# Kernel optimization log

Hardware: AMD Instinct MI355X
Metric: run time of the kernel (lower is better)

Reference implementation:

```python
import jax, jax.numpy as jnp
import numpy as np

N_NODES = 100000
N_EDGES = 3200000
N_FEAT = 512
N_HID = 256
N_CLASS = 40
K_HOPS = 10


def setup_inputs() -> dict:
    key = jax.random.key(0)
    ks = jax.random.split(key, 8)
    feature = jax.random.normal(ks[0], (N_NODES, N_FEAT), dtype=jnp.float32)
    edge_row = jax.random.randint(ks[1], (N_EDGES,), 0, N_NODES, dtype=jnp.int32)
    edge_col = jax.random.randint(ks[2], (N_EDGES,), 0, N_NODES, dtype=jnp.int32)
    edge_weight = jax.random.uniform(ks[3], (N_EDGES,), dtype=jnp.float32)
    W1 = jax.random.normal(ks[4], (N_FEAT, N_HID), dtype=jnp.float32) * (1.0 / np.sqrt(N_FEAT))
    b1 = jnp.zeros((N_HID,), dtype=jnp.float32)
    W2 = jax.random.normal(ks[5], (N_HID, N_CLASS), dtype=jnp.float32) * (1.0 / np.sqrt(N_HID))
    b2 = jnp.zeros((N_CLASS,), dtype=jnp.float32)
    Wa = jax.random.normal(ks[6], (N_CLASS, 1), dtype=jnp.float32) * (1.0 / np.sqrt(N_CLASS))
    ba = jnp.zeros((1,), dtype=jnp.float32)
    return {"feature": feature, "edge_row": edge_row, "edge_col": edge_col,
            "edge_weight": edge_weight, "W1": W1, "b1": b1, "W2": W2, "b2": b2,
            "Wa": Wa, "ba": ba}


def reference(feature, edge_row, edge_col, edge_weight, W1, b1, W2, b2, Wa, ba):
    # eval mode: dropout is identity
    x = jax.nn.relu(feature @ W1 + b1)          # [N, H]
    x = x @ W2 + b2                              # [N, C]
    # k-hop sparse propagation: out[i] = sum_e w_e * x[col_e] for row_e == i
    xs = [x]
    for _ in range(K_HOPS):
        x = jax.ops.segment_sum(edge_weight[:, None] * x[edge_col], edge_row,
                                num_segments=N_NODES)
        xs.append(x)
    xs = jnp.stack(xs, axis=1)                   # [N, K+1, C]
    score = jax.nn.sigmoid(jnp.squeeze(xs @ Wa + ba, -1))  # [N, K+1]
    out = jnp.einsum('nk,nkc->nc', score, xs)    # attention-weighted hop sum
    return jax.nn.log_softmax(out, axis=1)
```

## Files before the change

kernel.cpp:

```cpp
#include <hip/hip_runtime.h>
#include <math.h>

#define N_NODES 100000
#define N_EDGES 3200000
#define N_FEAT  512
#define N_HID   256
#define N_CLASS 40
#define K_HOPS  10

#define CAP        80
#define NGROUP     8
#define ROWS_PER_G (N_NODES / NGROUP)

typedef __attribute__((ext_vector_type(8))) short short8;
typedef __attribute__((ext_vector_type(8))) unsigned short ushort8v;
typedef __attribute__((ext_vector_type(4))) float float4v;

__device__ inline short f2bf(float f)
{
    union { float f; unsigned u; } v; v.f = f;
    unsigned r = v.u + 0x7FFF + ((v.u >> 16) & 1);
    return (short)(r >> 16);
}

__device__ inline float bf2f(unsigned short u)
{
    union { unsigned u; float f; } v; v.u = (unsigned)u << 16;
    return v.f;
}

__global__ void pack_w1(const float* __restrict__ W1, short* __restrict__ W1p)
{
    const int id = blockIdx.x * 256 + threadIdx.x;
    const int kb = id >> 8, n = id & 255;
    short tmp[32];
#pragma unroll
    for (int kl = 0; kl < 32; ++kl)
        tmp[kl] = f2bf(W1[(size_t)(kb * 32 + kl) * N_HID + n]);
    short8* dst = (short8*)&W1p[id * 32];
#pragma unroll
    for (int j = 0; j < 4; ++j) dst[j] = *(short8*)&tmp[j * 8];
}

__global__ void pack_w2(const float* __restrict__ W2, short* __restrict__ W2p)
{
    const int id = blockIdx.x * 256 + threadIdx.x;
    if (id >= 8 * 48) return;
    const int kb = id / 48, n = id % 48;
    short tmp[32];
#pragma unroll
    for (int kl = 0; kl < 32; ++kl)
        tmp[kl] = (n < N_CLASS) ? f2bf(W2[(size_t)(kb * 32 + kl) * N_CLASS + n]) : (short)0;
    short8* dst = (short8*)&W2p[id * 32];
#pragma unroll
    for (int j = 0; j < 4; ++j) dst[j] = *(short8*)&tmp[j * 8];
}

__global__ __launch_bounds__(256) void mlp_mfma(
    const float* __restrict__ feat, const short* __restrict__ W1p,
    const float* __restrict__ b1, const short* __restrict__ W2p,
    const float* __restrict__ b2, unsigned short* __restrict__ x0)
{
    __shared__ __align__(16) short smem[64 * 264];
    short (*As)[40]  = (short(*)[40])smem;
    short (*Hs)[264] = (short(*)[264])smem;

    const int t    = threadIdx.x;
    const int wave = t >> 6;
    const int lane = t & 63;
    const int q    = lane >> 4;
    const int m    = lane & 15;
    const int n0   = blockIdx.x * 64;
    const int colbase = wave * 64;

    float4v acc[4][4];
#pragma unroll
    for (int i = 0; i < 4; ++i)
#pragma unroll
        for (int j = 0; j < 4; ++j) acc[i][j] = (float4v)0.f;

    for (int kb = 0; kb < 16; ++kb) {
        const int k0 = kb * 32;
        __syncthreads();
        {
            const int r  = t >> 2;
            const int kq = t & 3;
            const int n  = n0 + r;
            float f[8];
            if (n < N_NODES) {
                const float* p = &feat[(size_t)n * N_FEAT + k0 + 8 * kq];
                float4 v0 = *(const float4*)p;
                float4 v1 = *(const float4*)(p + 4);
                f[0]=v0.x; f[1]=v0.y; f[2]=v0.z; f[3]=v0.w;
                f[4]=v1.x; f[5]=v1.y; f[6]=v1.z; f[7]=v1.w;
            } else {
#pragma unroll
                for (int j = 0; j < 8; ++j) f[j] = 0.f;
            }
            short8 st;
#pragma unroll
            for (int j = 0; j < 8; ++j) st[j] = f2bf(f[j]);
            *(short8*)&As[r][8 * kq] = st;
        }
        __syncthreads();

        short8 af[4], bfr[4];
#pragma unroll
        for (int rt = 0; rt < 4; ++rt)
            af[rt] = *(const short8*)&As[rt * 16 + m][q * 8];
#pragma unroll
        for (int ct = 0; ct < 4; ++ct) {
            const int off = (kb * 256 + colbase + ct * 16 + m) * 32 + q * 8;
            bfr[ct] = *(const short8*)&W1p[off];
        }
#pragma unroll
        for (int rt = 0; rt < 4; ++rt)
#pragma unroll
            for (int ct = 0; ct < 4; ++ct)
                acc[rt][ct] = __builtin_amdgcn_mfma_f32_16x16x32_bf16(
                    af[rt], bfr[ct], acc[rt][ct], 0, 0, 0);
    }

    __syncthreads();
#pragma unroll
    for (int ct = 0; ct < 4; ++ct) {
        const int col = colbase + ct * 16 + m;
        const float bias = b1[col];
#pragma unroll
        for (int rt = 0; rt < 4; ++rt) {
            const float4v d = acc[rt][ct];
#pragma unroll
            for (int r = 0; r < 4; ++r) {
                const float hv = fmaxf(d[r] + bias, 0.f);
                Hs[rt * 16 + q * 4 + r][col] = f2bf(hv);
            }
        }
    }
    __syncthreads();

    float4v acc2[3];
#pragma unroll
    for (int ct = 0; ct < 3; ++ct) acc2[ct] = (float4v)0.f;
#pragma unroll
    for (int kb = 0; kb < 8; ++kb) {
        const short8 a2 = *(const short8*)&Hs[wave * 16 + m][kb * 32 + q * 8];
#pragma unroll
        for (int ct = 0; ct < 3; ++ct) {
            const int off = (kb * 48 + ct * 16 + m) * 32 + q * 8;
            const short8 b2f = *(const short8*)&W2p[off];
            acc2[ct] = __builtin_amdgcn_mfma_f32_16x16x32_bf16(a2, b2f, acc2[ct], 0, 0, 0);
        }
    }
#pragma unroll
    for (int ct = 0; ct < 3; ++ct) {
        const int col = ct * 16 + m;
        if (col < N_CLASS) {
            const float bias = b2[col];
#pragma unroll
            for (int r = 0; r < 4; ++r) {
                const int row = n0 + wave * 16 + q * 4 + r;
                if (row < N_NODES)
                    x0[(size_t)row * N_CLASS + col] = (unsigned short)f2bf(acc2[ct][r] + bias);
            }
        }
    }
}

__global__ __launch_bounds__(256) void build_kernel(
    const int* __restrict__ erow, const int* __restrict__ ecol,
    const float* __restrict__ ew, int* __restrict__ cnt,
    unsigned int* __restrict__ ebuck)
{
    const int g     = blockIdx.x & 7;
    const int chunk = blockIdx.x >> 3;
    const int t     = chunk * 256 + threadIdx.x;
    const int base  = t * 16;
    if (base >= N_EDGES) return;
    const int rlo = g * ROWS_PER_G;

#pragma unroll
    for (int qv = 0; qv < 4; ++qv) {
        const int4 r = *(const int4*)&erow[base + qv * 4];
        const int rr[4] = {r.x, r.y, r.z, r.w};
#pragma unroll
        for (int j = 0; j < 4; ++j) {
            const unsigned d = (unsigned)(rr[j] - rlo);
            if (d < (unsigned)ROWS_PER_G) {
                const int   i   = base + qv * 4 + j;
                const int   col = ecol[i];
                const float w   = ew[i];
                int w15 = (int)(w * 32767.f + 0.5f);
                if (w15 > 32767) w15 = 32767;
                const unsigned rec = ((unsigned)w15 << 17) | (unsigned)col;
                const int pos = atomicAdd(&cnt[rr[j]], 1);
                if (pos < CAP)
                    ebuck[(size_t)rr[j] * CAP + pos] = rec;
            }
        }
    }
}

__device__ inline float wave_sum(float v)
{
#pragma unroll
    for (int o = 32; o; o >>= 1) v += __shfl_xor(v, o);
    return v;
}

__global__ __launch_bounds__(256) void attend0_kernel(
    const unsigned short* __restrict__ x, const float* __restrict__ Wa,
    const float* __restrict__ ba, float* __restrict__ acc)
{
    const int lane = threadIdx.x & 63;
    const int row  = blockIdx.x * 4 + (threadIdx.x >> 6);
    if (row >= N_NODES) return;
    const int  c   = lane;
    const bool act = c < N_CLASS;
    const float v  = act ? bf2f(x[(size_t)row * N_CLASS + c]) : 0.f;
    const float tt = act ? v * Wa[c] : 0.f;
    const float z  = wave_sum(tt) + ba[0];
    const float sc = 1.f / (1.f + expf(-z));
    if (act) acc[(size_t)row * N_CLASS + c] = sc * v;
}

__global__ __launch_bounds__(256) void hop_kernel(
    const int* __restrict__ cnt, const unsigned int* __restrict__ ebuck,
    const unsigned short* __restrict__ xin,
    unsigned short* __restrict__ xout, float* __restrict__ acc,
    const float* __restrict__ Wa, const float* __restrict__ ba)
{
    const int lane = threadIdx.x & 63;
    const int row  = blockIdx.x * 4 + (threadIdx.x >> 6);
    if (row >= N_NODES) return;
    const int  slot = lane >> 3;
    const int  l    = lane & 7;
    const bool act  = l < 5;

    int n = cnt[row];
    if (n > CAP) n = CAP;
    const size_t ebase = (size_t)row * CAP;

    unsigned rec_a = (lane < n) ? ebuck[ebase + lane] : 0u;

    float s[8];
#pragma unroll
    for (int j = 0; j < 8; ++j) s[j] = 0.f;

    const int nmain = (n < 64) ? n : 64;
    for (int e = 0; e < nmain; e += 8) {
        const unsigned r = __shfl(rec_a, e + slot);
        const int   col  = (int)(r & 0x1FFFFu);
        const float w    = (float)(r >> 17) * (1.f / 32767.f);
        if (act) {
            const ushort8v v = *(const ushort8v*)&xin[(size_t)col * N_CLASS + l * 8];
#pragma unroll
            for (int j = 0; j < 8; ++j) s[j] += w * bf2f(v[j]);
        }
    }
    for (int e = 64; e < n; e += 8) {
        const int ee = e + slot;
        unsigned r = 0u;
        if (ee < n) r = ebuck[ebase + ee];
        const int   col = (int)(r & 0x1FFFFu);
        const float w   = (float)(r >> 17) * (1.f / 32767.f);
        if (act) {
            const ushort8v v = *(const ushort8v*)&xin[(size_t)col * N_CLASS + l * 8];
#pragma unroll
            for (int j = 0; j < 8; ++j) s[j] += w * bf2f(v[j]);
        }
    }

#pragma unroll
    for (int o = 8; o <= 32; o <<= 1)
#pragma unroll
        for (int j = 0; j < 8; ++j) s[j] += __shfl_xor(s[j], o);

    float tq = 0.f;
    if (act) {
#pragma unroll
        for (int j = 0; j < 8; ++j) tq += s[j] * Wa[l * 8 + j];
    }
#pragma unroll
    for (int o = 1; o <= 4; o <<= 1) tq += __shfl_xor(tq, o);
    const float z  = tq + ba[0];
    const float sc = 1.f / (1.f + expf(-z));

    if (act && slot == 0) {
        ushort8v ov;
#pragma unroll
        for (int j = 0; j < 8; ++j) ov[j] = (unsigned short)f2bf(s[j]);
        *(ushort8v*)&xout[(size_t)row * N_CLASS + l * 8] = ov;

        float4* ap0 = (float4*)&acc[(size_t)row * N_CLASS + l * 8];
        float4 a0 = ap0[0];
        float4 a1 = ap0[1];
        a0.x += sc * s[0]; a0.y += sc * s[1]; a0.z += sc * s[2]; a0.w += sc * s[3];
        a1.x += sc * s[4]; a1.y += sc * s[5]; a1.z += sc * s[6]; a1.w += sc * s[7];
        ap0[0] = a0;
        ap0[1] = a1;
    }
}

__global__ __launch_bounds__(256) void logsoftmax_kernel(
    const float* __restrict__ acc, float* __restrict__ out)
{
    const int lane = threadIdx.x & 63;
    const int row  = blockIdx.x * 4 + (threadIdx.x >> 6);
    if (row >= N_NODES) return;
    const int  c   = lane;
    const bool act = c < N_CLASS;

    float v = act ? acc[(size_t)row * N_CLASS + c] : -INFINITY;
    float mx = v;
#pragma unroll
    for (int o = 32; o; o >>= 1) mx = fmaxf(mx, __shfl_xor(mx, o));
    const float e = act ? expf(v - mx) : 0.f;
    const float s = wave_sum(e);
    if (act) out[(size_t)row * N_CLASS + c] = v - mx - logf(s);
}

extern "C" void kernel_launch(void* const* d_in, const int* in_sizes, int n_in,
                              void* d_out, int out_size, void* d_ws, size_t ws_size,
                              hipStream_t stream)
{
    (void)in_sizes; (void)n_in; (void)out_size; (void)ws_size;
    const float* feat = (const float*)d_in[0];
    const int*   erow = (const int*)d_in[1];
    const int*   ecol = (const int*)d_in[2];
    const float* ew   = (const float*)d_in[3];
    const float* W1   = (const float*)d_in[4];
    const float* b1   = (const float*)d_in[5];
    const float* W2   = (const float*)d_in[6];
    const float* b2   = (const float*)d_in[7];
    const float* Wa   = (const float*)d_in[8];
    const float* ba   = (const float*)d_in[9];
    float* out = (float*)d_out;

    char* ws = (char*)d_ws;
    size_t off = 0;
    auto take = [&](size_t bytes) -> char* {
        char* p = ws + off;
        off += (bytes + 255) & ~(size_t)255;
        return p;
    };
    unsigned short* xb0 = (unsigned short*)take((size_t)N_NODES * N_CLASS * 2 + 64);
    unsigned short* xb1 = (unsigned short*)take((size_t)N_NODES * N_CLASS * 2 + 64);
    float*        acc   = (float*)take((size_t)N_NODES * N_CLASS * 4);
    int*          cnt   = (int*)take((size_t)N_NODES * 4);
    short*        W1p   = (short*)take((size_t)N_FEAT * N_HID * 2);
    short*        W2p   = (short*)take((size_t)N_HID * 48 * 2);
    unsigned int* ebuck = (unsigned int*)take((size_t)N_NODES * CAP * 4);

    hipMemsetAsync(cnt, 0, (size_t)N_NODES * 4, stream);

    pack_w1<<<16, 256, 0, stream>>>(W1, W1p);
    pack_w2<<<2, 256, 0, stream>>>(W2, W2p);
    mlp_mfma<<<(N_NODES + 63) / 64, 256, 0, stream>>>(feat, W1p, b1, W2p, b2, xb0);

    const int nchunk = (N_EDGES / 16 + 255) / 256;
    build_kernel<<<NGROUP * nchunk, 256, 0, stream>>>(erow, ecol, ew, cnt, ebuck);

    attend0_kernel<<<N_NODES / 4, 256, 0, stream>>>(xb0, Wa, ba, acc);

    const unsigned short* xin = xb0;
    unsigned short* xout = xb1;
    for (int k = 0; k < K_HOPS; ++k) {
        hop_kernel<<<N_NODES / 4, 256, 0, stream>>>(cnt, ebuck, xin, xout, acc, Wa, ba);
        unsigned short* tmp = (unsigned short*)xin;
        xin  = xout;
        xout = tmp;
    }

    logsoftmax_kernel<<<N_NODES / 4, 256, 0, stream>>>(acc, out);
}
```

Measured before the change: 1.257 ms.

## Replace grouped edge bucketing with two-pass row-bin sort and fuse hop-0 attention

The single build kernel, which rescanned all edges eight times, is replaced by a two-pass binning scheme. The first pass sorts each 4096-edge chunk in shared memory by coarse row bin and writes records contiguously into per-bin global buffers. The second pass scatters each bin into per-row buckets, so the per-row atomics and writes land in a localized region. The hop-0 attention score and accumulator initialization are folded into the MLP epilogue, removing a separate kernel and a reread of x0. The cost is an extra 8-byte-per-edge intermediate buffer and an extra kernel, and edges beyond a fixed bin capacity (BINCAP) would be silently dropped.

```diff
diff --git a/kernel.cpp b/kernel.cpp
--- a/kernel.cpp
+++ b/kernel.cpp
@@ -9,12 +9,19 @@
 #define K_HOPS  10
 
 #define CAP        80
-#define NGROUP     8
-#define ROWS_PER_G (N_NODES / NGROUP)
+
+#define BIN_SHIFT  11
+#define NBIN       49
+#define NBIN_PAD   56
+#define BINCAP     68000
+#define CHUNK1     4096
+#define CHUNK2     4096
+#define CPB2       17
 
 typedef __attribute__((ext_vector_type(8))) short short8;
 typedef __attribute__((ext_vector_type(8))) unsigned short ushort8v;
 typedef __attribute__((ext_vector_type(4))) float float4v;
+typedef unsigned long long u64;
 
 __device__ inline short f2bf(float f)
 {
@@ -59,7 +66,9 @@
 __global__ __launch_bounds__(256) void mlp_mfma(
     const float* __restrict__ feat, const short* __restrict__ W1p,
     const float* __restrict__ b1, const short* __restrict__ W2p,
-    const float* __restrict__ b2, unsigned short* __restrict__ x0)
+    const float* __restrict__ b2, const float* __restrict__ Wa,
+    const float* __restrict__ ba,
+    unsigned short* __restrict__ x0, float* __restrict__ acc_out)
 {
     __shared__ __align__(16) short smem[64 * 264];
     short (*As)[40]  = (short(*)[40])smem;
@@ -151,76 +160,151 @@
             acc2[ct] = __builtin_amdgcn_mfma_f32_16x16x32_bf16(a2, b2f, acc2[ct], 0, 0, 0);
         }
     }
+
+    float val[3][4];
 #pragma unroll
     for (int ct = 0; ct < 3; ++ct) {
         const int col = ct * 16 + m;
-        if (col < N_CLASS) {
-            const float bias = b2[col];
+        const bool cok = col < N_CLASS;
+        const float bias = cok ? b2[col] : 0.f;
+#pragma unroll
+        for (int r = 0; r < 4; ++r) val[ct][r] = acc2[ct][r] + bias;
+        if (cok) {
 #pragma unroll
             for (int r = 0; r < 4; ++r) {
                 const int row = n0 + wave * 16 + q * 4 + r;
                 if (row < N_NODES)
-                    x0[(size_t)row * N_CLASS + col] = (unsigned short)f2bf(acc2[ct][r] + bias);
+                    x0[(size_t)row * N_CLASS + col] = (unsigned short)f2bf(val[ct][r]);
             }
         }
     }
-}
-
-__global__ __launch_bounds__(256) void build_kernel(
+    float part[4];
+#pragma unroll
+    for (int r = 0; r < 4; ++r) {
+        float p = 0.f;
+#pragma unroll
+        for (int ct = 0; ct < 3; ++ct) {
+            const int col = ct * 16 + m;
+            if (col < N_CLASS) p += val[ct][r] * Wa[col];
+        }
+        part[r] = p;
+    }
+#pragma unroll
+    for (int o = 1; o <= 8; o <<= 1)
+#pragma unroll
+        for (int r = 0; r < 4; ++r) part[r] += __shfl_xor(part[r], o);
+    const float bb = ba[0];
+#pragma unroll
+    for (int r = 0; r < 4; ++r) {
+        const int row = n0 + wave * 16 + q * 4 + r;
+        if (row < N_NODES) {
+            const float sc = 1.f / (1.f + expf(-(part[r] + bb)));
+#pragma unroll
+            for (int ct = 0; ct < 3; ++ct) {
+                const int col = ct * 16 + m;
+                if (col < N_CLASS)
+                    acc_out[(size_t)row * N_CLASS + col] = sc * val[ct][r];
+            }
+        }
+    }
+}
+
+__global__ __launch_bounds__(256) void bin_kernel(
     const int* __restrict__ erow, const int* __restrict__ ecol,
-    const float* __restrict__ ew, int* __restrict__ cnt,
-    unsigned int* __restrict__ ebuck)
-{
-    const int g     = blockIdx.x & 7;
-    const int chunk = blockIdx.x >> 3;
-    const int t     = chunk * 256 + threadIdx.x;
-    const int base  = t * 16;
-    if (base >= N_EDGES) return;
-    const int rlo = g * ROWS_PER_G;
-
-#pragma unroll
-    for (int qv = 0; qv < 4; ++qv) {
-        const int4 r = *(const int4*)&erow[base + qv * 4];
-        const int rr[4] = {r.x, r.y, r.z, r.w};
-#pragma unroll
-        for (int j = 0; j < 4; ++j) {
-            const unsigned d = (unsigned)(rr[j] - rlo);
-            if (d < (unsigned)ROWS_PER_G) {
-                const int   i   = base + qv * 4 + j;
-                const int   col = ecol[i];
-                const float w   = ew[i];
-                int w15 = (int)(w * 32767.f + 0.5f);
-                if (w15 > 32767) w15 = 32767;
-                const unsigned rec = ((unsigned)w15 << 17) | (unsigned)col;
-                const int pos = atomicAdd(&cnt[rr[j]], 1);
-                if (pos < CAP)
-                    ebuck[(size_t)rr[j] * CAP + pos] = rec;
+    const float* __restrict__ ew, int* __restrict__ bin_cursor,
+    u64* __restrict__ bins)
+{
+    __shared__ __align__(16) u64 recs[CHUNK1];
+    __shared__ int hist[NBIN], h2[NBIN], lbase[NBIN], adj[NBIN];
+
+    const int t     = threadIdx.x;
+    const int cbase = blockIdx.x * CHUNK1;
+    const int e0    = cbase + t * 16;
+    const bool has  = e0 < N_EDGES;
+    const int chunk_n = min(CHUNK1, N_EDGES - cbase);
+
+    for (int i = t; i < NBIN; i += 256) { hist[i] = 0; h2[i] = 0; }
+    __syncthreads();
+
+    int   rows[16], cols[16], w15[16];
+    if (has) {
+#pragma unroll
+        for (int qv = 0; qv < 4; ++qv) {
+            const int4   r = *(const int4*)&erow[e0 + qv * 4];
+            const int4   c = *(const int4*)&ecol[e0 + qv * 4];
+            const float4 w = *(const float4*)&ew[e0 + qv * 4];
+            rows[qv*4+0]=r.x; rows[qv*4+1]=r.y; rows[qv*4+2]=r.z; rows[qv*4+3]=r.w;
+            cols[qv*4+0]=c.x; cols[qv*4+1]=c.y; cols[qv*4+2]=c.z; cols[qv*4+3]=c.w;
+            const float wf[4] = {w.x, w.y, w.z, w.w};
+#pragma unroll
+            for (int j = 0; j < 4; ++j) {
+                int v = (int)(wf[j] * 32767.f + 0.5f);
+                w15[qv*4+j] = (v > 32767) ? 32767 : v;
             }
         }
-    }
-}
-
-__device__ inline float wave_sum(float v)
-{
-#pragma unroll
-    for (int o = 32; o; o >>= 1) v += __shfl_xor(v, o);
-    return v;
-}
-
-__global__ __launch_bounds__(256) void attend0_kernel(
-    const unsigned short* __restrict__ x, const float* __restrict__ Wa,
-    const float* __restrict__ ba, float* __restrict__ acc)
-{
-    const int lane = threadIdx.x & 63;
-    const int row  = blockIdx.x * 4 + (threadIdx.x >> 6);
-    if (row >= N_NODES) return;
-    const int  c   = lane;
-    const bool act = c < N_CLASS;
-    const float v  = act ? bf2f(x[(size_t)row * N_CLASS + c]) : 0.f;
-    const float tt = act ? v * Wa[c] : 0.f;
-    const float z  = wave_sum(tt) + ba[0];
-    const float sc = 1.f / (1.f + expf(-z));
-    if (act) acc[(size_t)row * N_CLASS + c] = sc * v;
+#pragma unroll
+        for (int j = 0; j < 16; ++j)
+            atomicAdd(&hist[rows[j] >> BIN_SHIFT], 1);
+    }
+    __syncthreads();
+
+    if (t == 0) {
+        int run = 0;
+        for (int b = 0; b < NBIN; ++b) { lbase[b] = run; run += hist[b]; }
+    }
+    __syncthreads();
+    if (t < NBIN) {
+        const int g = atomicAdd(&bin_cursor[t], hist[t]);
+        adj[t] = g - lbase[t];
+    }
+    __syncthreads();
+
+    if (has) {
+#pragma unroll
+        for (int j = 0; j < 16; ++j) {
+            const int b = rows[j] >> BIN_SHIFT;
+            const int p = lbase[b] + atomicAdd(&h2[b], 1);
+            recs[p] = ((u64)w15[j] << 34) | ((u64)rows[j] << 17) | (u64)cols[j];
+        }
+    }
+    __syncthreads();
+
+    for (int i = t; i < chunk_n; i += 256) {
+        const u64 r   = recs[i];
+        const int row = (int)((r >> 17) & 0x1FFFF);
+        const int b   = row >> BIN_SHIFT;
+        const int di  = adj[b] + i;
+        if (di < BINCAP)
+            bins[(size_t)b * BINCAP + di] = r;
+    }
+}
+
+__global__ __launch_bounds__(256) void scatter_bins(
+    const int* __restrict__ bin_cursor, const u64* __restrict__ bins,
+    int* __restrict__ cnt, unsigned int* __restrict__ ebuck)
+{
+    const int b = blockIdx.x % NBIN_PAD;
+    if (b >= NBIN) return;
+    const int chunk = blockIdx.x / NBIN_PAD;
+    int n = bin_cursor[b];
+    if (n > BINCAP) n = BINCAP;
+    const int start = chunk * CHUNK2;
+    if (start >= n) return;
+    const u64* src = &bins[(size_t)b * BINCAP];
+
+#pragma unroll
+    for (int j = 0; j < 16; ++j) {
+        const int idx = start + j * 256 + threadIdx.x;
+        if (idx < n) {
+            const u64 r   = src[idx];
+            const int col = (int)(r & 0x1FFFF);
+            const int row = (int)((r >> 17) & 0x1FFFF);
+            const unsigned rec = ((unsigned)(r >> 34) << 17) | (unsigned)col;
+            const int pos = atomicAdd(&cnt[row], 1);
+            if (pos < CAP)
+                ebuck[(size_t)row * CAP + pos] = rec;
+        }
+    }
 }
 
 __global__ __launch_bounds__(256) void hop_kernel(
@@ -299,6 +383,13 @@
         ap0[0] = a0;
         ap0[1] = a1;
     }
+}
+
+__device__ inline float wave_sum(float v)
+{
+#pragma unroll
+    for (int o = 32; o; o >>= 1) v += __shfl_xor(v, o);
+    return v;
 }
 
 __global__ __launch_bounds__(256) void logsoftmax_kernel(
@@ -347,20 +438,23 @@
     unsigned short* xb1 = (unsigned short*)take((size_t)N_NODES * N_CLASS * 2 + 64);
     float*        acc   = (float*)take((size_t)N_NODES * N_CLASS * 4);
     int*          cnt   = (int*)take((size_t)N_NODES * 4);
+    int*          bcur  = (int*)take((size_t)NBIN_PAD * 4);
     short*        W1p   = (short*)take((size_t)N_FEAT * N_HID * 2);
     short*        W2p   = (short*)take((size_t)N_HID * 48 * 2);
     unsigned int* ebuck = (unsigned int*)take((size_t)N_NODES * CAP * 4);
+    u64*          bins  = (u64*)take((size_t)NBIN * BINCAP * 8);
 
     hipMemsetAsync(cnt, 0, (size_t)N_NODES * 4, stream);
+    hipMemsetAsync(bcur, 0, (size_t)NBIN_PAD * 4, stream);
 
     pack_w1<<<16, 256, 0, stream>>>(W1, W1p);
     pack_w2<<<2, 256, 0, stream>>>(W2, W2p);
-    mlp_mfma<<<(N_NODES + 63) / 64, 256, 0, stream>>>(feat, W1p, b1, W2p, b2, xb0);
-
-    const int nchunk = (N_EDGES / 16 + 255) / 256;
-    build_kernel<<<NGROUP * nchunk, 256, 0, stream>>>(erow, ecol, ew, cnt, ebuck);
-
-    attend0_kernel<<<N_NODES / 4, 256, 0, stream>>>(xb0, Wa, ba, acc);
+    mlp_mfma<<<(N_NODES + 63) / 64, 256, 0, stream>>>(feat, W1p, b1, W2p, b2,
+                                                      Wa, ba, xb0, acc);
+
+    const int nchunk1 = (N_EDGES + CHUNK1 - 1) / CHUNK1;
+    bin_kernel<<<nchunk1, 256, 0, stream>>>(erow, ecol, ew, bcur, bins);
+    scatter_bins<<<NBIN_PAD * CPB2, 256, 0, stream>>>(bcur, bins, cnt, ebuck);
 
     const unsigned short* xin = xb0;
     unsigned short* xout = xb1;
```

Measured after the change: 1.174 ms. 1.07x faster.
